# Kernel optimization log

Hardware: AMD Instinct MI355X
Metric: run time of the kernel (lower is better)

The kernel has to match this reference:

```python
import jax, jax.numpy as jnp
import numpy as np
import math

B, S, D, H, HD, W, G = 2, 4096, 768, 12, 64, 256, 64  # batch, seq, embed, heads, head_dim, one-sided window, n global tokens


def _chunk_keys(k, w):
    # k: [B,S,H,HD] -> overlapping 3w-wide key windows per w-sized query chunk: [B,nc,3w,H,HD]
    Bz, S_, Hh, HDd = k.shape
    nc = S_ // w
    kp = jnp.pad(k, ((0, 0), (w, w), (0, 0), (0, 0)))
    kb = kp.reshape(Bz, nc + 2, w, Hh, HDd)
    return jnp.concatenate([kb[:, 0:nc], kb[:, 1:nc + 1], kb[:, 2:nc + 2]], axis=2)


def _band_qk(q, k, w):
    # banded scores: out[b,i,h,j] = q_i . k_{i+j-w}, j in [0, 2w]
    Bz, S_, Hh, HDd = q.shape
    nc = S_ // w
    qc = q.reshape(Bz, nc, w, Hh, HDd)
    kc = _chunk_keys(k, w)
    sc = jnp.einsum('bcphd,bckhd->bchpk', qc, kc)  # [B,nc,H,w,3w]
    rows = jnp.arange(w)[:, None]
    cols = rows + jnp.arange(2 * w + 1)[None, :]   # within-window key index = p + j
    band = sc[:, :, :, rows, cols]                 # [B,nc,H,w,2w+1]
    return band.transpose(0, 1, 3, 2, 4).reshape(Bz, S_, Hh, 2 * w + 1)


def _band_pv(p, v, w):
    # out[b,i,h,:] = sum_j p[b,i,h,j] * v[b, i+j-w, h, :]
    Bz, S_, Hh, K = p.shape
    HDd = v.shape[-1]
    nc = S_ // w
    pc = p.reshape(Bz, nc, w, Hh, K).transpose(0, 1, 3, 2, 4)  # [B,nc,H,w,2w+1]
    rows = jnp.arange(w)[:, None]
    cols = rows + jnp.arange(2 * w + 1)[None, :]
    full = jnp.zeros((Bz, nc, Hh, w, 3 * w), p.dtype).at[:, :, :, rows, cols].set(pc)
    vc = _chunk_keys(v, w)
    out = jnp.einsum('bchpk,bckhd->bcphd', full, vc)  # [B,nc,w,H,HD]
    return out.reshape(Bz, S_, Hh, HDd)


def setup_inputs() -> dict:
    key = jax.random.key(0)
    ks = jax.random.split(key, 4)
    std = 0.02
    # attention mask: +1 = global (first G tokens), 0 = local windowed, no padding
    attention_mask = jnp.concatenate(
        [jnp.ones((B, G), jnp.int32), jnp.zeros((B, S - G), jnp.int32)], axis=1)
    return {
        'hidden_states': jax.random.normal(ks[0], (B, S, D), jnp.float32),
        'attention_mask': attention_mask,
        'Wq': jax.random.normal(ks[1], (D, D), jnp.float32) * std,
        'bq': jnp.zeros((D,), jnp.float32),
        'Wk': jax.random.normal(ks[2], (D, D), jnp.float32) * std,
        'bk': jnp.zeros((D,), jnp.float32),
        'Wv': jax.random.normal(ks[3], (D, D), jnp.float32) * std,
        'bv': jnp.zeros((D,), jnp.float32),
    }


def reference(hidden_states, attention_mask, Wq, bq, Wk, bk, Wv, bv):
    Bz, S_, D_ = hidden_states.shape
    HDd = D_ // H
    q = ((hidden_states @ Wq.T + bq) / math.sqrt(HDd)).reshape(Bz, S_, H, HDd)
    k = (hidden_states @ Wk.T + bk).reshape(Bz, S_, H, HDd)
    v = (hidden_states @ Wv.T + bv).reshape(Bz, S_, H, HDd)

    band = _band_qk(q, k, W)  # [B,S,H,2W+1]

    i = jnp.arange(S_)
    key_abs = i[:, None] + jnp.arange(2 * W + 1)[None, :] - W  # [S,2W+1]
    valid = (key_abs >= 0) & (key_abs < S_)
    kac = jnp.clip(key_abs, 0, S_ - 1)
    is_glob = attention_mask != 0                       # [B,S]
    glob_at_key = is_glob[:, kac] & valid[None]          # [B,S,2W+1]
    # remove global keys from windowed attention: d_mask = -10000 * head_dim (ones @ float_mask)
    band = band + jnp.where(glob_at_key, jnp.float32(-10000.0 * HDd), jnp.float32(0.0))[:, :, None, :]
    # mask_invalid_locations: out-of-range diagonals -> -inf
    band = jnp.where(valid[None, :, None, :], band, -jnp.inf)

    # global-token attention (first G tokens are the global ones)
    gs = jnp.einsum('bihd,bghd->bihg', q, k[:, :G])      # [B,S,H,G]

    scores = jnp.concatenate([gs, band], axis=-1)        # [B,S,H,G+2W+1]
    probs = jax.nn.softmax(scores.astype(jnp.float32), axis=-1)

    attn = jnp.einsum('bihg,bghd->bihd', probs[..., :G], v[:, :G]) + _band_pv(probs[..., G:], v, W)
    # [B,S,H,HD] -> (seq_len, bsz, embed_dim) as in the torch module
    return jnp.transpose(attn, (1, 0, 2, 3)).reshape(S_, Bz, D_)
```

## Files before the change

### kernel.cpp

```cpp
#include <hip/hip_runtime.h>
#include <hip/hip_bf16.h>
#include <stdint.h>

typedef __attribute__((ext_vector_type(4))) float          f32x4;
typedef __attribute__((ext_vector_type(4))) float          f4;
typedef __attribute__((ext_vector_type(2))) unsigned int   u32x2;
typedef __bf16 bf16_t;
typedef __attribute__((ext_vector_type(8))) bf16_t         bf16x8;
typedef __attribute__((ext_vector_type(8))) unsigned short u16x8;
typedef __attribute__((ext_vector_type(4))) unsigned short u16x4;

#define NB 2
#define NS 4096
#define ND 768
#define NH 12
#define NW 256

__device__ __forceinline__ unsigned short f2bf(float f) {
  union { float f; unsigned u; } v; v.f = f;
  unsigned r = v.u + 0x7fffu + ((v.u >> 16) & 1u);
  return (unsigned short)(r >> 16);
}

__device__ __forceinline__ void gload16(const void* g, void* l) {
  __builtin_amdgcn_global_load_lds((const __attribute__((address_space(1))) void*)g,
                                   (__attribute__((address_space(3))) void*)l, 16, 0, 0);
}

__global__ void cast_kernel(const float* __restrict__ in, unsigned short* __restrict__ out, int n4) {
  int i = blockIdx.x * blockDim.x + threadIdx.x;
  int stride = gridDim.x * blockDim.x;
  for (; i < n4; i += stride) {
    f4 v = reinterpret_cast<const f4*>(in)[i];
    unsigned u0 = (unsigned)f2bf(v.x) | ((unsigned)f2bf(v.y) << 16);
    unsigned u1 = (unsigned)f2bf(v.z) | ((unsigned)f2bf(v.w) << 16);
    u32x2 o = {u0, u1};
    reinterpret_cast<u32x2*>(out)[i] = o;
  }
}

__global__ void cast3_kernel(const float* __restrict__ w0, const float* __restrict__ w1,
                             const float* __restrict__ w2, unsigned short* __restrict__ o0,
                             unsigned short* __restrict__ o1, unsigned short* __restrict__ o2) {
  const int n4 = 768 * 768 / 4;
  int i = blockIdx.x * blockDim.x + threadIdx.x;
  int stride = gridDim.x * blockDim.x;
  for (; i < 3 * n4; i += stride) {
    int m = i / n4, j = i - m * n4;
    const float* in = (m == 0) ? w0 : ((m == 1) ? w1 : w2);
    unsigned short* out = (m == 0) ? o0 : ((m == 1) ? o1 : o2);
    f4 v = reinterpret_cast<const f4*>(in)[j];
    unsigned u0 = (unsigned)f2bf(v.x) | ((unsigned)f2bf(v.y) << 16);
    unsigned u1 = (unsigned)f2bf(v.z) | ((unsigned)f2bf(v.w) << 16);
    u32x2 o = {u0, u1};
    reinterpret_cast<u32x2*>(out)[j] = o;
  }
}

__global__ __launch_bounds__(256) void qkv_gemm(
    const unsigned short* __restrict__ Ab,
    const unsigned short* __restrict__ Wqb,
    const unsigned short* __restrict__ Wkb,
    const unsigned short* __restrict__ Wvb,
    const float* __restrict__ bqp, const float* __restrict__ bkp, const float* __restrict__ bvp,
    unsigned short* __restrict__ Qw, unsigned short* __restrict__ Kw, unsigned short* __restrict__ Vw) {
  __shared__ unsigned short As[128 * 32];
  __shared__ unsigned short Bs[128 * 32];

  int phys = blockIdx.x;
  int logical = (phys & 7) * 144 + (phys >> 3);
  int bn = logical % 18, bm = logical / 18;
  int mat = bn / 6, bnn = bn % 6;
  const unsigned short* Wm = (mat == 0) ? Wqb : ((mat == 1) ? Wkb : Wvb);
  const float* bias = (mat == 0) ? bqp : ((mat == 1) ? bkp : bvp);
  unsigned short* dst = (mat == 0) ? Qw : ((mat == 1) ? Kw : Vw);

  int t = threadIdx.x;
  int w = t >> 6, l = t & 63;
  int lg = l >> 4, ln = l & 15;
  int wm = w & 1, wn = w >> 1;

  f32x4 acc[4][4];
#pragma unroll
  for (int i = 0; i < 4; i++)
#pragma unroll
    for (int j = 0; j < 4; j++) acc[i][j] = f32x4{0.f, 0.f, 0.f, 0.f};

  for (int kt = 0; kt < 24; ++kt) {
    __syncthreads();
#pragma unroll
    for (int is = 0; is < 2; ++is) {
      int chunk = is * 256 + t;
      int row = chunk >> 2;
      int c8 = (chunk & 3) * 8;
      gload16(Ab + ((size_t)(bm * 128 + row)) * 768 + kt * 32 + c8, As + chunk * 8);
      gload16(Wm + ((size_t)(bnn * 128 + row)) * 768 + kt * 32 + c8, Bs + chunk * 8);
    }
    __syncthreads();
    bf16x8 af[4], bfr[4];
#pragma unroll
    for (int i = 0; i < 4; i++) {
      af[i]  = *reinterpret_cast<const bf16x8*>(As + (wm * 64 + i * 16 + ln) * 32 + lg * 8);
      bfr[i] = *reinterpret_cast<const bf16x8*>(Bs + (wn * 64 + i * 16 + ln) * 32 + lg * 8);
    }
#pragma unroll
    for (int i = 0; i < 4; i++)
#pragma unroll
      for (int j = 0; j < 4; j++)
        acc[i][j] = __builtin_amdgcn_mfma_f32_16x16x32_bf16(af[i], bfr[j], acc[i][j], 0, 0, 0);
  }

#pragma unroll
  for (int j = 0; j < 4; j++) {
    int col = bnn * 128 + wn * 64 + j * 16 + ln;
    float bv_ = bias[col];
    int hh = col >> 6, dd = col & 63;
#pragma unroll
    for (int i = 0; i < 4; i++) {
#pragma unroll
      for (int r = 0; r < 4; r++) {
        int tok = bm * 128 + wm * 64 + i * 16 + lg * 4 + r;
        int bb = tok >> 12, ss = tok & 4095;
        float v = acc[i][j][r] + bv_;
        if (mat == 0) v *= 0.125f;
        dst[(((size_t)bb * 12 + hh) * 4096 + ss) * 64 + dd] = f2bf(v);
      }
    }
  }
}

__global__ __launch_bounds__(512) void attn_kernel(
    const unsigned short* __restrict__ Qw,
    const unsigned short* __restrict__ Kw,
    const unsigned short* __restrict__ Vw,
    const int* __restrict__ amask,
    float* __restrict__ out) {
  __shared__ unsigned short Ks[64 * 64];
  __shared__ unsigned short Vt[64 * 64];
  __shared__ unsigned short Ps[8][16 * 72];

  int phys = blockIdx.x;
  int logical = (phys & 7) * 96 + (phys >> 3);
  int qc = logical & 31;
  int bh = logical >> 5;
  int b = bh / 12;
  int hh = bh % 12;
  int qbase = qc * 128;

  int t = threadIdx.x, w = t >> 6, l = t & 63;
  int lg = l >> 4, ln = l & 15;

  const unsigned short* Qbh = Qw + (size_t)bh * (NS * 64);
  const unsigned short* Kbh = Kw + (size_t)bh * (NS * 64);
  const unsigned short* Vbh = Vw + (size_t)bh * (NS * 64);
  const int* mrow = amask + b * NS;

  bf16x8 qf[2];
  {
    const unsigned short* qp = Qbh + (size_t)(qbase + w * 16 + ln) * 64 + lg * 8;
    qf[0] = *reinterpret_cast<const bf16x8*>(qp);
    qf[1] = *reinterpret_cast<const bf16x8*>(qp + 32);
  }

  float m_r[4] = {-1e30f, -1e30f, -1e30f, -1e30f};
  float l_r[4] = {0.f, 0.f, 0.f, 0.f};
  f32x4 oacc[4];
#pragma unroll
  for (int i = 0; i < 4; i++) oacc[i] = f32x4{0.f, 0.f, 0.f, 0.f};

  int q0 = qbase + w * 16 + lg * 4;

  for (int tt = -1; tt < 10; ++tt) {
    int key0 = (tt < 0) ? 0 : (qbase - 256 + tt * 64);
    if (key0 < 0 || key0 >= NS) continue;

    __syncthreads();
    {
      int krow = t >> 3, gran = t & 7;
      gload16(Kbh + (size_t)(key0 + krow) * 64 + (gran ^ (krow & 7)) * 8, Ks + t * 8);
    }
    {
      int p2 = t & 31;
      int d0 = (t >> 5) * 4;
      const unsigned short* vp0 = Vbh + (size_t)(key0 + 2 * p2) * 64 + d0;
      u16x4 va = *reinterpret_cast<const u16x4*>(vp0);
      u16x4 vb = *reinterpret_cast<const u16x4*>(vp0 + 64);
#pragma unroll
      for (int j = 0; j < 4; ++j) {
        int d = d0 + j;
        unsigned val = (unsigned)va[j] | ((unsigned)vb[j] << 16);
        *reinterpret_cast<unsigned*>(Vt + d * 64 + ((2 * p2) ^ ((d & 7) << 3))) = val;
      }
    }
    __syncthreads();

    f32x4 sa[4];
#pragma unroll
    for (int nt = 0; nt < 4; nt++) sa[nt] = f32x4{0.f, 0.f, 0.f, 0.f};
#pragma unroll
    for (int nt = 0; nt < 4; nt++) {
      int key = nt * 16 + ln;
#pragma unroll
      for (int ks = 0; ks < 2; ++ks) {
        int dby = (ks * 64 + lg * 16) ^ ((key & 7) << 4);
        bf16x8 kf = *reinterpret_cast<const bf16x8*>(Ks + key * 64 + (dby >> 1));
        sa[nt] = __builtin_amdgcn_mfma_f32_16x16x32_bf16(qf[ks], kf, sa[nt], 0, 0, 0);
      }
    }

    if (tt >= 0) {
#pragma unroll
      for (int nt = 0; nt < 4; nt++) {
        int ka = key0 + nt * 16 + ln;
        int sup = mrow[ka];
#pragma unroll
        for (int r = 0; r < 4; r++) {
          int qa = q0 + r;
          bool ok = (sup == 0) && (ka >= qa - NW) && (ka <= qa + NW);
          if (!ok) sa[nt][r] = -1e30f;
        }
      }
    }

    float scl[4];
#pragma unroll
    for (int r = 0; r < 4; r++) {
      float v = fmaxf(fmaxf(sa[0][r], sa[1][r]), fmaxf(sa[2][r], sa[3][r]));
      v = fmaxf(v, __shfl_xor(v, 1, 64));
      v = fmaxf(v, __shfl_xor(v, 2, 64));
      v = fmaxf(v, __shfl_xor(v, 4, 64));
      v = fmaxf(v, __shfl_xor(v, 8, 64));
      float mn = fmaxf(m_r[r], v);
      scl[r] = __expf(m_r[r] - mn);
      m_r[r] = mn;
    }
#pragma unroll
    for (int r = 0; r < 4; r++) {
      float s = 0.f;
#pragma unroll
      for (int nt = 0; nt < 4; nt++) {
        float p = __expf(sa[nt][r] - m_r[r]);
        sa[nt][r] = p;
        s += p;
      }
      s += __shfl_xor(s, 1, 64);
      s += __shfl_xor(s, 2, 64);
      s += __shfl_xor(s, 4, 64);
      s += __shfl_xor(s, 8, 64);
      l_r[r] = l_r[r] * scl[r] + s;
    }
#pragma unroll
    for (int nt = 0; nt < 4; nt++)
#pragma unroll
      for (int r = 0; r < 4; r++) oacc[nt][r] *= scl[r];

    unsigned short* pw = &Ps[w][0];
#pragma unroll
    for (int nt = 0; nt < 4; nt++)
#pragma unroll
      for (int r = 0; r < 4; r++)
        pw[(lg * 4 + r) * 72 + nt * 16 + ln] = f2bf(sa[nt][r]);

#pragma unroll
    for (int ks = 0; ks < 2; ++ks) {
      bf16x8 pf = *reinterpret_cast<const bf16x8*>(pw + ln * 72 + ks * 32 + lg * 8);
#pragma unroll
      for (int nt = 0; nt < 4; ++nt) {
        int d = nt * 16 + ln;
        int eoff = (ks * 32 + lg * 8) ^ ((d & 7) << 3);
        bf16x8 vf = *reinterpret_cast<const bf16x8*>(Vt + d * 64 + eoff);
        oacc[nt] = __builtin_amdgcn_mfma_f32_16x16x32_bf16(pf, vf, oacc[nt], 0, 0, 0);
      }
    }
  }

#pragma unroll
  for (int nt = 0; nt < 4; nt++) {
    int d = nt * 16 + ln;
#pragma unroll
    for (int r = 0; r < 4; r++) {
      int qa = q0 + r;
      out[((size_t)qa * NB + b) * ND + hh * 64 + d] = oacc[nt][r] / l_r[r];
    }
  }
}

extern "C" void kernel_launch(void* const* d_in, const int* in_sizes, int n_in,
                              void* d_out, int out_size, void* d_ws, size_t ws_size,
                              hipStream_t stream) {
  (void)in_sizes; (void)n_in; (void)out_size; (void)ws_size;
  const float* hidden = (const float*)d_in[0];
  const int*   amask  = (const int*)d_in[1];
  const float* Wq = (const float*)d_in[2];
  const float* bq = (const float*)d_in[3];
  const float* Wk = (const float*)d_in[4];
  const float* bk = (const float*)d_in[5];
  const float* Wv = (const float*)d_in[6];
  const float* bv = (const float*)d_in[7];
  float* out = (float*)d_out;

  char* p = (char*)d_ws;
  unsigned short* hb  = (unsigned short*)p; p += (size_t)8192 * 768 * 2;
  unsigned short* wqb = (unsigned short*)p; p += (size_t)768 * 768 * 2;
  unsigned short* wkb = (unsigned short*)p; p += (size_t)768 * 768 * 2;
  unsigned short* wvb = (unsigned short*)p; p += (size_t)768 * 768 * 2;
  unsigned short* Qws = (unsigned short*)p; p += (size_t)24 * 4096 * 64 * 2;
  unsigned short* Kws = (unsigned short*)p; p += (size_t)24 * 4096 * 64 * 2;
  unsigned short* Vws = (unsigned short*)p; p += (size_t)24 * 4096 * 64 * 2;

  cast_kernel<<<1024, 256, 0, stream>>>(hidden, hb, 8192 * 768 / 4);
  cast3_kernel<<<432, 256, 0, stream>>>(Wq, Wk, Wv, wqb, wkb, wvb);
  qkv_gemm<<<64 * 18, 256, 0, stream>>>(hb, wqb, wkb, wvb, bq, bk, bv, Qws, Kws, Vws);
  attn_kernel<<<24 * 32, 512, 0, stream>>>(Qws, Kws, Vws, amask, out);
}
```

Before: 212.5 us.

## Double-buffer K/V tiles and precompute global mask bits in shared memory

The attention loop now keeps two shared-memory buffers for K and V, so the next tile's loads are issued before the current tile's QK and PV work and its V-transpose stores happen afterwards. This drops one barrier per iteration and hides global load latency. The attention mask is ballot-compressed into a shared bitmask at kernel start, which replaces per-key global mask loads, and the loop bounds are computed up front instead of skipping invalid tiles. The cost is twice the shared memory for K/V, which may lower occupancy, plus a swap to the library bf16 conversion.

```diff
diff --git a/kernel.cpp b/kernel.cpp
--- a/kernel.cpp
+++ b/kernel.cpp
@@ -135,9 +135,10 @@
     const unsigned short* __restrict__ Vw,
     const int* __restrict__ amask,
     float* __restrict__ out) {
-  __shared__ unsigned short Ks[64 * 64];
-  __shared__ unsigned short Vt[64 * 64];
+  __shared__ unsigned short Ks[2][64 * 64];
+  __shared__ unsigned short Vt[2][64 * 64];
   __shared__ unsigned short Ps[8][16 * 72];
+  __shared__ unsigned Msk[128];
 
   int phys = blockIdx.x;
   int logical = (phys & 7) * 96 + (phys >> 3);
@@ -155,6 +156,16 @@
   const unsigned short* Vbh = Vw + (size_t)bh * (NS * 64);
   const int* mrow = amask + b * NS;
 
+#pragma unroll
+  for (int r8 = 0; r8 < 8; ++r8) {
+    int wp = r8 * 8 + w;
+    unsigned long long bal = __ballot(mrow[wp * 64 + l] != 0);
+    if (l == 0) {
+      Msk[wp * 2] = (unsigned)bal;
+      Msk[wp * 2 + 1] = (unsigned)(bal >> 32);
+    }
+  }
+
   bf16x8 qf[2];
   {
     const unsigned short* qp = Qbh + (size_t)(qbase + w * 16 + ln) * 64 + lg * 8;
@@ -170,30 +181,44 @@
 
   int q0 = qbase + w * 16 + lg * 4;
 
-  for (int tt = -1; tt < 10; ++tt) {
-    int key0 = (tt < 0) ? 0 : (qbase - 256 + tt * 64);
-    if (key0 < 0 || key0 >= NS) continue;
-
-    __syncthreads();
-    {
-      int krow = t >> 3, gran = t & 7;
-      gload16(Kbh + (size_t)(key0 + krow) * 64 + (gran ^ (krow & 7)) * 8, Ks + t * 8);
-    }
-    {
-      int p2 = t & 31;
-      int d0 = (t >> 5) * 4;
-      const unsigned short* vp0 = Vbh + (size_t)(key0 + 2 * p2) * 64 + d0;
-      u16x4 va = *reinterpret_cast<const u16x4*>(vp0);
-      u16x4 vb = *reinterpret_cast<const u16x4*>(vp0 + 64);
-#pragma unroll
-      for (int j = 0; j < 4; ++j) {
-        int d = d0 + j;
-        unsigned val = (unsigned)va[j] | ((unsigned)vb[j] << 16);
-        *reinterpret_cast<unsigned*>(Vt + d * 64 + ((2 * p2) ^ ((d & 7) << 3))) = val;
-      }
-    }
-    __syncthreads();
-
+  int tt_lo = (qbase >= 256) ? 0 : ((256 - qbase) >> 6);
+  int tt_hi_raw = (NS + 192 - qbase) >> 6;
+  int tt_hi = tt_hi_raw < 9 ? tt_hi_raw : 9;
+  int ntl = tt_hi - tt_lo + 2;
+
+  int krow = t >> 3, gran = t & 7;
+  int p2 = t & 31, d0v = (t >> 5) * 4;
+
+  {
+    gload16(Kbh + (size_t)krow * 64 + (gran ^ (krow & 7)) * 8, &Ks[0][0] + t * 8);
+    const unsigned short* vp0 = Vbh + (size_t)(2 * p2) * 64 + d0v;
+    u16x4 va = *reinterpret_cast<const u16x4*>(vp0);
+    u16x4 vb = *reinterpret_cast<const u16x4*>(vp0 + 64);
+#pragma unroll
+    for (int j = 0; j < 4; ++j) {
+      int d = d0v + j;
+      unsigned val = (unsigned)va[j] | ((unsigned)vb[j] << 16);
+      *reinterpret_cast<unsigned*>(&Vt[0][0] + d * 64 + ((2 * p2) ^ ((d & 7) << 3))) = val;
+    }
+  }
+  __syncthreads();
+
+  for (int idx = 0; idx < ntl; ++idx) {
+    int cur = idx & 1;
+    int key0 = (idx == 0) ? 0 : (qbase - 256 + (tt_lo + idx - 1) * 64);
+    bool has_next = (idx + 1) < ntl;
+
+    u16x4 va, vb;
+    if (has_next) {
+      int nk0 = qbase - 256 + (tt_lo + idx) * 64;
+      gload16(Kbh + (size_t)(nk0 + krow) * 64 + (gran ^ (krow & 7)) * 8,
+              &Ks[cur ^ 1][0] + t * 8);
+      const unsigned short* vp0 = Vbh + (size_t)(nk0 + 2 * p2) * 64 + d0v;
+      va = *reinterpret_cast<const u16x4*>(vp0);
+      vb = *reinterpret_cast<const u16x4*>(vp0 + 64);
+    }
+
+    const unsigned short* ksb = &Ks[cur][0];
     f32x4 sa[4];
 #pragma unroll
     for (int nt = 0; nt < 4; nt++) sa[nt] = f32x4{0.f, 0.f, 0.f, 0.f};
@@ -203,21 +228,20 @@
 #pragma unroll
       for (int ks = 0; ks < 2; ++ks) {
         int dby = (ks * 64 + lg * 16) ^ ((key & 7) << 4);
-        bf16x8 kf = *reinterpret_cast<const bf16x8*>(Ks + key * 64 + (dby >> 1));
+        bf16x8 kf = *reinterpret_cast<const bf16x8*>(ksb + key * 64 + (dby >> 1));
         sa[nt] = __builtin_amdgcn_mfma_f32_16x16x32_bf16(qf[ks], kf, sa[nt], 0, 0, 0);
       }
     }
 
-    if (tt >= 0) {
+    if (idx > 0) {
 #pragma unroll
       for (int nt = 0; nt < 4; nt++) {
         int ka = key0 + nt * 16 + ln;
-        int sup = mrow[ka];
+        bool sup = (Msk[ka >> 5] >> (ka & 31)) & 1;
 #pragma unroll
         for (int r = 0; r < 4; r++) {
-          int qa = q0 + r;
-          bool ok = (sup == 0) && (ka >= qa - NW) && (ka <= qa + NW);
-          if (!ok) sa[nt][r] = -1e30f;
+          bool bad = sup || ((unsigned)(ka - (q0 + r) + NW) > 2u * NW);
+          if (bad) sa[nt][r] = -1e30f;
         }
       }
     }
@@ -258,9 +282,12 @@
 #pragma unroll
     for (int nt = 0; nt < 4; nt++)
 #pragma unroll
-      for (int r = 0; r < 4; r++)
-        pw[(lg * 4 + r) * 72 + nt * 16 + ln] = f2bf(sa[nt][r]);
-
+      for (int r = 0; r < 4; r++) {
+        __hip_bfloat16 hb = __float2bfloat16(sa[nt][r]);
+        pw[(lg * 4 + r) * 72 + nt * 16 + ln] = *reinterpret_cast<unsigned short*>(&hb);
+      }
+
+    const unsigned short* vtb = &Vt[cur][0];
 #pragma unroll
     for (int ks = 0; ks < 2; ++ks) {
       bf16x8 pf = *reinterpret_cast<const bf16x8*>(pw + ln * 72 + ks * 32 + lg * 8);
@@ -268,10 +295,21 @@
       for (int nt = 0; nt < 4; ++nt) {
         int d = nt * 16 + ln;
         int eoff = (ks * 32 + lg * 8) ^ ((d & 7) << 3);
-        bf16x8 vf = *reinterpret_cast<const bf16x8*>(Vt + d * 64 + eoff);
+        bf16x8 vf = *reinterpret_cast<const bf16x8*>(vtb + d * 64 + eoff);
         oacc[nt] = __builtin_amdgcn_mfma_f32_16x16x32_bf16(pf, vf, oacc[nt], 0, 0, 0);
       }
     }
+
+    if (has_next) {
+      unsigned short* vtn = &Vt[cur ^ 1][0];
+#pragma unroll
+      for (int j = 0; j < 4; ++j) {
+        int d = d0v + j;
+        unsigned val = (unsigned)va[j] | ((unsigned)vb[j] << 16);
+        *reinterpret_cast<unsigned*>(vtn + d * 64 + ((2 * p2) ^ ((d & 7) << 3))) = val;
+      }
+    }
+    __syncthreads();
   }
 
 #pragma unroll
```

Result: no change. 209.7 us (-1.3%).
